# Performance work log

Hardware: AMD Instinct MI355X
Metric: run time of the kernel (lower is better)

Reference implementation:

```python
import jax, jax.numpy as jnp
import numpy as np

SCALE_FACTOR = 2  # init kwarg
KERNEL = 1        # kernel=1 -> no Gaussian inpainting of empty cells
EPS = 1e-6


def token2map_agg(x, loc_orig, idx_agg, H, W):
    """Scatter-average aggregated tokens onto a dense [B,C,H,W] map.

    Faithful to token2map_agg_sparse with weight=None, kernel=1:
      each original position i gets feature x[idx_agg[i]] with weight 1,
      scattered to the grid cell of loc_orig[i]; per-cell average with
      denominator (count + 1e-6).
    """
    B, N, C = x.shape
    N0 = loc_orig.shape[1]
    lo = jnp.clip(loc_orig, -1.0, 1.0)
    wh = jnp.array([W, H], dtype=lo.dtype)
    # normalized [-1,1] -> pixel coords, round-half-even like torch.round
    px = jnp.round(0.5 * (lo + 1.0) * wh - 0.5).astype(jnp.int32)
    ix = jnp.clip(px[..., 0], 0, W - 1)
    iy = jnp.clip(px[..., 1], 0, H - 1)
    seg = (iy * W + ix + jnp.arange(B, dtype=jnp.int32)[:, None] * (H * W)).reshape(-1)  # [B*N0]
    # gather token feature for each original position: [B, N0, C]
    feats = jnp.take_along_axis(x, idx_agg[..., None].astype(jnp.int32), axis=1)
    # scatter features and counts together in one segment_sum
    src = jnp.concatenate([feats, jnp.ones_like(feats[..., :1])], axis=-1).reshape(B * N0, C + 1)
    agg = jax.ops.segment_sum(src, seg, num_segments=B * H * W)  # [B*H*W, C+1]
    out = agg[:, :C] / (agg[:, C:] + EPS)
    return out.reshape(B, H, W, C).transpose(0, 3, 1, 2)  # [B,C,H,W]


def setup_inputs() -> dict:
    key = jax.random.key(0)
    k1, k2, k3, k4 = jax.random.split(key, 4)
    B, N, C = 8, 1024, 128
    N0 = 16384  # 128*128 original grid positions
    x = jax.random.normal(k1, (B, N, C), dtype=jnp.float32)
    loc = jax.random.uniform(k2, (B, N, 2), dtype=jnp.float32, minval=-1.0, maxval=1.0)
    loc_orig = jax.random.uniform(k3, (B, N0, 2), dtype=jnp.float32, minval=-1.0, maxval=1.0)
    idx_agg = jax.random.randint(k4, (B, N0), 0, N, dtype=jnp.int32)
    return {"x": x, "loc": loc, "loc_orig": loc_orig, "idx_agg": idx_agg,
            "map_h": 128, "map_w": 128}


def reference(x, loc, loc_orig, idx_agg, map_h, map_w):
    B, N, C = x.shape
    N0 = idx_agg.shape[1]
    scale_orig = (N0 // N) ** 0.5  # static python value
    if SCALE_FACTOR <= scale_orig:
        h, w = int(map_h * SCALE_FACTOR), int(map_w * SCALE_FACTOR)
        out = token2map_agg(x, loc_orig, idx_agg, h, w)
    else:
        h, w = int(map_h * scale_orig), int(map_w * scale_orig)
        out = token2map_agg(x, loc_orig, idx_agg, h, w)
        h, w = int(map_h * SCALE_FACTOR), int(map_w * SCALE_FACTOR)
        out = jax.image.resize(out, (B, C, h, w), method="bilinear")
    return out
```

## Files before the change

### kernel.cpp

```cpp
#include <hip/hip_runtime.h>

constexpr int B  = 8;
constexpr int N  = 1024;
constexpr int C  = 128;
constexpr int N0 = 16384;
constexpr int HH = 256;
constexpr int WW = 256;
constexpr int HW = HH * WW;
constexpr int NPTS = B * N0;

constexpr int CPG    = 256;
constexpr int GPB    = HW / CPG;
constexpr int NGRP   = B * GPB;
constexpr int CSPLIT = 4;
constexpr int CHB    = C / CSPLIT;
constexpr int CAP    = 192;

constexpr int ROWW = CPG + 4;
constexpr int ACC_WORDS = CHB * ROWW;

__device__ __forceinline__ int cell_of(float lx, float ly) {
    lx = fminf(fmaxf(lx, -1.0f), 1.0f);
    ly = fminf(fmaxf(ly, -1.0f), 1.0f);
    float pxf = rintf(0.5f * (lx + 1.0f) * 256.0f - 0.5f);
    float pyf = rintf(0.5f * (ly + 1.0f) * 256.0f - 0.5f);
    int ix = (int)pxf; ix = ix < 0 ? 0 : (ix > WW - 1 ? WW - 1 : ix);
    int iy = (int)pyf; iy = iy < 0 ? 0 : (iy > HH - 1 ? HH - 1 : iy);
    return iy * WW + ix;
}

__global__ void bucket_kernel(const float* __restrict__ loc_orig,
                              const int* __restrict__ idx_agg,
                              int* __restrict__ cursor,
                              int* __restrict__ bucket) {
    int p = blockIdx.x * blockDim.x + threadIdx.x;
    if (p >= NPTS) return;
    float2 l = ((const float2*)loc_orig)[p];
    int b = p >> 14;
    int cell = cell_of(l.x, l.y);
    int g = b * GPB + (cell >> 8);
    int pos = atomicAdd(cursor + g, 1);
    if (pos < CAP) bucket[g * CAP + pos] = ((cell & 255) << 10) | idx_agg[p];
}

__global__ __launch_bounds__(512) void gather_kernel(
        const float* __restrict__ x,
        const int* __restrict__ cursor,
        const int* __restrict__ bucket,
        float* __restrict__ out) {
    __shared__ __align__(16) float acc[ACC_WORDS];
    __shared__ __align__(16) float scale[CPG];
    __shared__ int recs[CAP];
    __shared__ int cnt_s;

    int gid    = blockIdx.x;
    int bgrp   = gid & (NGRP - 1);
    int csplit = gid >> 11;
    int b      = bgrp >> 8;
    int cell0  = (bgrp & 255) * CPG;
    int ch0    = csplit * CHB;
    int tid    = threadIdx.x;
    int wave   = tid >> 6, lane = tid & 63;

    int my_cnt = (tid == 0) ? cursor[bgrp] : 0;
    int my_rec = (tid < CAP) ? bucket[bgrp * CAP + tid] : 0;

    float4 z4 = make_float4(0.f, 0.f, 0.f, 0.f);
    for (int i = tid; i < ACC_WORDS / 4; i += 512) ((float4*)acc)[i] = z4;
    for (int i = tid; i < CPG / 4; i += 512) ((float4*)scale)[i] = z4;
    if (tid == 0) cnt_s = my_cnt > CAP ? CAP : my_cnt;
    if (tid < CAP) recs[tid] = my_rec;
    __syncthreads();

    int cnt = cnt_s;
    int chl = lane & 15;
    const float* xb = x + (size_t)b * N * C + ch0;
    for (int base = wave * 4; base < cnt; base += 32) {
        int p = base + (lane >> 4);
        if (p < cnt) {
            int e = recs[p];
            int local = e >> 10;
            int tok   = e & 1023;
            float2 v = ((const float2*)(xb + (size_t)tok * C))[chl];
            atomicAdd(&acc[chl * ROWW + local],        v.x);
            atomicAdd(&acc[(chl + 16) * ROWW + local], v.y);
            if (chl == 0) atomicAdd(&scale[local], 1.0f);
        }
    }
    __syncthreads();
    for (int i = tid; i < CPG; i += 512) scale[i] = 1.0f / (scale[i] + 1e-6f);
    __syncthreads();

    int q  = tid & 63;
    int i4 = q * 4;
    int cl = tid >> 6;
    float4 s = *(const float4*)&scale[i4];
    float* obase = out + (size_t)b * C * HW + cell0;
    #pragma unroll
    for (int it = 0; it < 4; ++it) {
        int c  = it * 8 + cl;
        int rr = (c >> 1) + ((c & 1) << 4);
        float4 v = *(const float4*)&acc[rr * ROWW + i4];
        v.x *= s.x; v.y *= s.y; v.z *= s.z; v.w *= s.w;
        *(float4*)(obase + (size_t)(ch0 + c) * HW + i4) = v;
    }
}

extern "C" void kernel_launch(void* const* d_in, const int* in_sizes, int n_in,
                              void* d_out, int out_size, void* d_ws, size_t ws_size,
                              hipStream_t stream) {
    const float* x        = (const float*)d_in[0];
    const float* loc_orig = (const float*)d_in[2];
    const int*   idx_agg  = (const int*)d_in[3];
    float* out = (float*)d_out;

    int* cursor = (int*)d_ws;
    int* bucket = cursor + NGRP;

    hipMemsetAsync(cursor, 0, NGRP * sizeof(int), stream);
    bucket_kernel<<<(NPTS + 255) / 256, 256, 0, stream>>>(loc_orig, idx_agg, cursor, bucket);
    gather_kernel<<<NGRP * CSPLIT, 512, 0, stream>>>(x, cursor, bucket, out);
}
```

Measured before the change: 342.4 us.

## Precompute per-cell counts in bucket pass, vectorize bucketing, use nontemporal stores

Each cell's point count is now computed once, with global atomics in the bucket kernel, instead of being recomputed by all four channel-split gather blocks through shared atomics. The bucket kernel handles two points per thread with vectorized loads, and the bucket and output writes use nontemporal stores. In exchange the memset grows to cover 512K per-cell counters and the bucket kernel does extra global atomics. Each gather block also reads the counts from global memory.

```diff
diff --git a/kernel.cpp b/kernel.cpp
--- a/kernel.cpp
+++ b/kernel.cpp
@@ -8,6 +8,7 @@
 constexpr int WW = 256;
 constexpr int HW = HH * WW;
 constexpr int NPTS = B * N0;
+constexpr int NCELL = B * HW;
 
 constexpr int CPG    = 256;
 constexpr int GPB    = HW / CPG;
@@ -18,6 +19,8 @@
 
 constexpr int ROWW = CPG + 4;
 constexpr int ACC_WORDS = CHB * ROWW;
+
+typedef float vfloat4 __attribute__((ext_vector_type(4)));
 
 __device__ __forceinline__ int cell_of(float lx, float ly) {
     lx = fminf(fmaxf(lx, -1.0f), 1.0f);
@@ -32,24 +35,37 @@
 __global__ void bucket_kernel(const float* __restrict__ loc_orig,
                               const int* __restrict__ idx_agg,
                               int* __restrict__ cursor,
+                              int* __restrict__ cellcnt,
                               int* __restrict__ bucket) {
-    int p = blockIdx.x * blockDim.x + threadIdx.x;
-    if (p >= NPTS) return;
-    float2 l = ((const float2*)loc_orig)[p];
-    int b = p >> 14;
-    int cell = cell_of(l.x, l.y);
-    int g = b * GPB + (cell >> 8);
-    int pos = atomicAdd(cursor + g, 1);
-    if (pos < CAP) bucket[g * CAP + pos] = ((cell & 255) << 10) | idx_agg[p];
+    int t = blockIdx.x * blockDim.x + threadIdx.x;
+    int p0 = t * 2;
+    if (p0 >= NPTS) return;
+    float4 l2 = ((const float4*)loc_orig)[t];
+    int2  ia  = ((const int2*)idx_agg)[t];
+    int b = p0 >> 14;
+    #pragma unroll
+    for (int k = 0; k < 2; ++k) {
+        float lx = k ? l2.z : l2.x;
+        float ly = k ? l2.w : l2.y;
+        int tok  = k ? ia.y : ia.x;
+        int cell = cell_of(lx, ly);
+        int gcell = b * HW + cell;
+        atomicAdd(cellcnt + gcell, 1);
+        int g = b * GPB + (cell >> 8);
+        int pos = atomicAdd(cursor + g, 1);
+        if (pos < CAP)
+            __builtin_nontemporal_store(((cell & 255) << 10) | tok,
+                                        bucket + g * CAP + pos);
+    }
 }
 
 __global__ __launch_bounds__(512) void gather_kernel(
         const float* __restrict__ x,
         const int* __restrict__ cursor,
+        const int* __restrict__ cellcnt,
         const int* __restrict__ bucket,
         float* __restrict__ out) {
     __shared__ __align__(16) float acc[ACC_WORDS];
-    __shared__ __align__(16) float scale[CPG];
     __shared__ int recs[CAP];
     __shared__ int cnt_s;
 
@@ -67,7 +83,6 @@
 
     float4 z4 = make_float4(0.f, 0.f, 0.f, 0.f);
     for (int i = tid; i < ACC_WORDS / 4; i += 512) ((float4*)acc)[i] = z4;
-    for (int i = tid; i < CPG / 4; i += 512) ((float4*)scale)[i] = z4;
     if (tid == 0) cnt_s = my_cnt > CAP ? CAP : my_cnt;
     if (tid < CAP) recs[tid] = my_rec;
     __syncthreads();
@@ -84,25 +99,28 @@
             float2 v = ((const float2*)(xb + (size_t)tok * C))[chl];
             atomicAdd(&acc[chl * ROWW + local],        v.x);
             atomicAdd(&acc[(chl + 16) * ROWW + local], v.y);
-            if (chl == 0) atomicAdd(&scale[local], 1.0f);
         }
     }
-    __syncthreads();
-    for (int i = tid; i < CPG; i += 512) scale[i] = 1.0f / (scale[i] + 1e-6f);
     __syncthreads();
 
     int q  = tid & 63;
     int i4 = q * 4;
     int cl = tid >> 6;
-    float4 s = *(const float4*)&scale[i4];
+    int4 c4 = *(const int4*)(cellcnt + b * HW + cell0 + i4);
+    float4 s;
+    s.x = 1.0f / ((float)c4.x + 1e-6f);
+    s.y = 1.0f / ((float)c4.y + 1e-6f);
+    s.z = 1.0f / ((float)c4.z + 1e-6f);
+    s.w = 1.0f / ((float)c4.w + 1e-6f);
     float* obase = out + (size_t)b * C * HW + cell0;
     #pragma unroll
     for (int it = 0; it < 4; ++it) {
         int c  = it * 8 + cl;
         int rr = (c >> 1) + ((c & 1) << 4);
         float4 v = *(const float4*)&acc[rr * ROWW + i4];
-        v.x *= s.x; v.y *= s.y; v.z *= s.z; v.w *= s.w;
-        *(float4*)(obase + (size_t)(ch0 + c) * HW + i4) = v;
+        vfloat4 nv = { v.x * s.x, v.y * s.y, v.z * s.z, v.w * s.w };
+        __builtin_nontemporal_store(nv,
+            (vfloat4*)(obase + (size_t)(ch0 + c) * HW + i4));
     }
 }
 
@@ -114,10 +132,12 @@
     const int*   idx_agg  = (const int*)d_in[3];
     float* out = (float*)d_out;
 
-    int* cursor = (int*)d_ws;
-    int* bucket = cursor + NGRP;
+    int* cursor  = (int*)d_ws;
+    int* cellcnt = cursor + NGRP;
+    int* bucket  = cellcnt + NCELL;
 
-    hipMemsetAsync(cursor, 0, NGRP * sizeof(int), stream);
-    bucket_kernel<<<(NPTS + 255) / 256, 256, 0, stream>>>(loc_orig, idx_agg, cursor, bucket);
-    gather_kernel<<<NGRP * CSPLIT, 512, 0, stream>>>(x, cursor, bucket, out);
+    (void)hipMemsetAsync(cursor, 0, (NGRP + NCELL) * sizeof(int), stream);
+    bucket_kernel<<<(NPTS / 2 + 255) / 256, 256, 0, stream>>>(loc_orig, idx_agg,
+                                                              cursor, cellcnt, bucket);
+    gather_kernel<<<NGRP * CSPLIT, 512, 0, stream>>>(x, cursor, cellcnt, bucket, out);
 }
```

Measured after the change: 348.2 us. Within noise of the previous version (+1.7%).

## Fuse memset, bucketing and gather into one cooperative persistent kernel

Applied to the files above, without the earlier changes.

Replaces the memset plus two kernel launches with a single cooperative kernel. It zeroes the cursors, buckets the points two per thread, and then runs the gather phase over virtual groups in a persistent loop, with grid-wide syncs between phases. The aim is to remove launch and inter-kernel gaps. In exchange it adds grid.sync costs, caps concurrency at occupancy-sized grids, and relies on the grid size hardcoded to 256 CUs.

```diff
diff --git a/kernel.cpp b/kernel.cpp
--- a/kernel.cpp
+++ b/kernel.cpp
@@ -1,4 +1,7 @@
 #include <hip/hip_runtime.h>
+#include <hip/hip_cooperative_groups.h>
+
+namespace cg = cooperative_groups;
 
 constexpr int B  = 8;
 constexpr int N  = 1024;
@@ -15,6 +18,7 @@
 constexpr int CSPLIT = 4;
 constexpr int CHB    = C / CSPLIT;
 constexpr int CAP    = 192;
+constexpr int NVG    = NGRP * CSPLIT;
 
 constexpr int ROWW = CPG + 4;
 constexpr int ACC_WORDS = CHB * ROWW;
@@ -29,80 +33,94 @@
     return iy * WW + ix;
 }
 
-__global__ void bucket_kernel(const float* __restrict__ loc_orig,
-                              const int* __restrict__ idx_agg,
-                              int* __restrict__ cursor,
-                              int* __restrict__ bucket) {
-    int p = blockIdx.x * blockDim.x + threadIdx.x;
-    if (p >= NPTS) return;
-    float2 l = ((const float2*)loc_orig)[p];
-    int b = p >> 14;
-    int cell = cell_of(l.x, l.y);
-    int g = b * GPB + (cell >> 8);
-    int pos = atomicAdd(cursor + g, 1);
-    if (pos < CAP) bucket[g * CAP + pos] = ((cell & 255) << 10) | idx_agg[p];
-}
-
-__global__ __launch_bounds__(512) void gather_kernel(
+__global__ __launch_bounds__(512) void fused_kernel(
         const float* __restrict__ x,
-        const int* __restrict__ cursor,
-        const int* __restrict__ bucket,
+        const float* __restrict__ loc_orig,
+        const int* __restrict__ idx_agg,
+        int* __restrict__ cursor,
+        int* __restrict__ bucket,
         float* __restrict__ out) {
     __shared__ __align__(16) float acc[ACC_WORDS];
     __shared__ __align__(16) float scale[CPG];
     __shared__ int recs[CAP];
     __shared__ int cnt_s;
 
-    int gid    = blockIdx.x;
-    int bgrp   = gid & (NGRP - 1);
-    int csplit = gid >> 11;
-    int b      = bgrp >> 8;
-    int cell0  = (bgrp & 255) * CPG;
-    int ch0    = csplit * CHB;
-    int tid    = threadIdx.x;
-    int wave   = tid >> 6, lane = tid & 63;
+    cg::grid_group grid = cg::this_grid();
+    int tid  = threadIdx.x;
+    int nthr = gridDim.x * 512;
+    int gtid = blockIdx.x * 512 + tid;
 
-    int my_cnt = (tid == 0) ? cursor[bgrp] : 0;
-    int my_rec = (tid < CAP) ? bucket[bgrp * CAP + tid] : 0;
+    for (int i = gtid; i < NGRP; i += nthr) cursor[i] = 0;
+    grid.sync();
 
-    float4 z4 = make_float4(0.f, 0.f, 0.f, 0.f);
-    for (int i = tid; i < ACC_WORDS / 4; i += 512) ((float4*)acc)[i] = z4;
-    for (int i = tid; i < CPG / 4; i += 512) ((float4*)scale)[i] = z4;
-    if (tid == 0) cnt_s = my_cnt > CAP ? CAP : my_cnt;
-    if (tid < CAP) recs[tid] = my_rec;
-    __syncthreads();
-
-    int cnt = cnt_s;
-    int chl = lane & 15;
-    const float* xb = x + (size_t)b * N * C + ch0;
-    for (int base = wave * 4; base < cnt; base += 32) {
-        int p = base + (lane >> 4);
-        if (p < cnt) {
-            int e = recs[p];
-            int local = e >> 10;
-            int tok   = e & 1023;
-            float2 v = ((const float2*)(xb + (size_t)tok * C))[chl];
-            atomicAdd(&acc[chl * ROWW + local],        v.x);
-            atomicAdd(&acc[(chl + 16) * ROWW + local], v.y);
-            if (chl == 0) atomicAdd(&scale[local], 1.0f);
+    for (int t = gtid; t < NPTS / 2; t += nthr) {
+        float4 l2 = ((const float4*)loc_orig)[t];
+        int2  ia  = ((const int2*)idx_agg)[t];
+        int b = (t * 2) >> 14;
+        #pragma unroll
+        for (int k = 0; k < 2; ++k) {
+            float lx = k ? l2.z : l2.x;
+            float ly = k ? l2.w : l2.y;
+            int tok  = k ? ia.y : ia.x;
+            int cell = cell_of(lx, ly);
+            int g = b * GPB + (cell >> 8);
+            int pos = atomicAdd(cursor + g, 1);
+            if (pos < CAP) bucket[g * CAP + pos] = ((cell & 255) << 10) | tok;
         }
     }
-    __syncthreads();
-    for (int i = tid; i < CPG; i += 512) scale[i] = 1.0f / (scale[i] + 1e-6f);
-    __syncthreads();
+    grid.sync();
 
-    int q  = tid & 63;
-    int i4 = q * 4;
-    int cl = tid >> 6;
-    float4 s = *(const float4*)&scale[i4];
-    float* obase = out + (size_t)b * C * HW + cell0;
-    #pragma unroll
-    for (int it = 0; it < 4; ++it) {
-        int c  = it * 8 + cl;
-        int rr = (c >> 1) + ((c & 1) << 4);
-        float4 v = *(const float4*)&acc[rr * ROWW + i4];
-        v.x *= s.x; v.y *= s.y; v.z *= s.z; v.w *= s.w;
-        *(float4*)(obase + (size_t)(ch0 + c) * HW + i4) = v;
+    int wave = tid >> 6, lane = tid & 63;
+    int chl  = lane & 15;
+    for (int vg = blockIdx.x; vg < NVG; vg += gridDim.x) {
+        int bgrp   = vg & (NGRP - 1);
+        int csplit = vg >> 11;
+        int b      = bgrp >> 8;
+        int cell0  = (bgrp & 255) * CPG;
+        int ch0    = csplit * CHB;
+
+        int my_cnt = (tid == 0) ? cursor[bgrp] : 0;
+        int my_rec = (tid < CAP) ? bucket[bgrp * CAP + tid] : 0;
+
+        float4 z4 = make_float4(0.f, 0.f, 0.f, 0.f);
+        for (int i = tid; i < ACC_WORDS / 4; i += 512) ((float4*)acc)[i] = z4;
+        if (tid < CPG) scale[tid] = 0.0f;
+        if (tid == 0) cnt_s = my_cnt > CAP ? CAP : my_cnt;
+        if (tid < CAP) recs[tid] = my_rec;
+        __syncthreads();
+
+        int cnt = cnt_s;
+        const float* xb = x + (size_t)b * N * C + ch0;
+        for (int base = wave * 4; base < cnt; base += 32) {
+            int p = base + (lane >> 4);
+            if (p < cnt) {
+                int e = recs[p];
+                int local = e >> 10;
+                int tok   = e & 1023;
+                float2 v = ((const float2*)(xb + (size_t)tok * C))[chl];
+                atomicAdd(&acc[chl * ROWW + local],        v.x);
+                atomicAdd(&acc[(chl + 16) * ROWW + local], v.y);
+                if (chl == 0) atomicAdd(&scale[local], 1.0f);
+            }
+        }
+        __syncthreads();
+        if (tid < CPG) scale[tid] = 1.0f / (scale[tid] + 1e-6f);
+        __syncthreads();
+
+        int q  = tid & 63;
+        int i4 = q * 4;
+        int cl = tid >> 6;
+        float4 s = *(const float4*)&scale[i4];
+        float* obase = out + (size_t)b * C * HW + cell0;
+        #pragma unroll
+        for (int it = 0; it < 4; ++it) {
+            int c  = it * 8 + cl;
+            int rr = (c >> 1) + ((c & 1) << 4);
+            float4 v = *(const float4*)&acc[rr * ROWW + i4];
+            v.x *= s.x; v.y *= s.y; v.z *= s.z; v.w *= s.w;
+            *(float4*)(obase + (size_t)(ch0 + c) * HW + i4) = v;
+        }
+        __syncthreads();
     }
 }
 
@@ -117,7 +135,14 @@
     int* cursor = (int*)d_ws;
     int* bucket = cursor + NGRP;
 
-    hipMemsetAsync(cursor, 0, NGRP * sizeof(int), stream);
-    bucket_kernel<<<(NPTS + 255) / 256, 256, 0, stream>>>(loc_orig, idx_agg, cursor, bucket);
-    gather_kernel<<<NGRP * CSPLIT, 512, 0, stream>>>(x, cursor, bucket, out);
+    int bpc = 0;
+    (void)hipOccupancyMaxActiveBlocksPerMultiprocessor(&bpc, fused_kernel, 512, 0);
+    if (bpc < 1) bpc = 1;
+    int grid = bpc * 256;
+    if (grid > NVG) grid = NVG;
+
+    void* args[] = {(void*)&x, (void*)&loc_orig, (void*)&idx_agg,
+                    (void*)&cursor, (void*)&bucket, (void*)&out};
+    (void)hipLaunchCooperativeKernel((void*)fused_kernel, dim3(grid), dim3(512),
+                                     args, 0, stream);
 }
```

Result: slower. 457.8 us (+33.7%).
